# Kernel optimization log

Hardware: AMD Instinct MI355X
Metric: run time of the kernel (lower is better)

Reference implementation:

```python
import jax, jax.numpy as jnp
import numpy as np

N = 16384      # nodes
E = 524288     # edges (avg degree 32)
F_IN = 128     # input features
H1 = 256       # first_gcn_dimensions
H2 = 256       # second_gcn_dimensions
D1 = 64        # first_dense_neurons
D2 = 2         # second_dense_neurons (fixed by EYE=ones(2))


def setup_inputs() -> dict:
    key = jax.random.key(0)
    ks = jax.random.split(key, 8)
    w = lambda k, shp: (jax.random.normal(k, shp, jnp.float32) * 0.05)
    return dict(
        features=jax.random.normal(ks[0], (N, F_IN), jnp.float32),
        edges=jax.random.randint(ks[1], (2, E), 0, N),
        W1=w(ks[2], (F_IN, H1)), b1=jnp.zeros((H1,), jnp.float32),
        W2=w(ks[3], (H1, H2)), b2=jnp.zeros((H2,), jnp.float32),
        fc1_w=w(ks[4], (D1, H2)), fc1_b=jnp.zeros((D1,), jnp.float32),
        fc2_w=w(ks[5], (D2, D1)), fc2_b=jnp.zeros((D2,), jnp.float32),
    )


def gcn_conv(x, W, b, src, dst, n):
    """PyG GCNConv: xW, add self-loops, symmetric D^-1/2 (A+I) D^-1/2 aggregation."""
    x = x @ W
    loops = jnp.arange(n)
    s = jnp.concatenate([src, loops])
    d = jnp.concatenate([dst, loops])
    deg = jax.ops.segment_sum(jnp.ones(s.shape, x.dtype), d, num_segments=n)
    dinv = jnp.where(deg > 0, jax.lax.rsqrt(deg), 0.0)
    msg = x[s] * (dinv[s] * dinv[d])[:, None]          # gather + scale
    return jax.ops.segment_sum(msg, d, num_segments=n) + b  # scatter-add


def reference(features, edges, W1, b1, W2, b2, fc1_w, fc1_b, fc2_w, fc2_b):
    n = features.shape[0]
    src, dst = edges[0], edges[1]
    h1 = jax.nn.relu(gcn_conv(features, W1, b1, src, dst, n))
    h2 = gcn_conv(h1, W2, b2, src, dst, n)                 # [N, H2]
    a1 = jnp.tanh(h2 @ fc1_w.T + fc1_b)                    # [N, D1]
    assignment = jax.nn.softmax(a1 @ fc2_w.T + fc2_b, axis=1)  # [N, 2]
    group_features = assignment.T @ h2                     # [2, H2]
    # to_dense_adj: dense NxN adjacency, duplicate edges accumulate
    adj = jnp.zeros((n, n), h2.dtype).at[src, dst].add(1.0)
    new_adj = assignment.T @ (adj @ assignment)            # [2, 2]
    positive = jnp.clip(group_features[0][None, :], -100.0, 100.0)
    negative = jnp.clip(group_features[1][None, :], -100.0, 100.0)
    # F.normalize(p=1, dim=1) with eps=1e-12
    denom = jnp.maximum(jnp.sum(jnp.abs(new_adj), axis=1, keepdims=True), 1e-12)
    norm_diag = jnp.diag(new_adj / denom)
    pos_penalty = jnp.mean((norm_diag - 1.0) ** 2)         # MSE vs ones(2)
    graph_embedding = jnp.mean(group_features, axis=0, keepdims=True)  # [1, H2]
    return (graph_embedding, positive, negative, pos_penalty)
```

## Files before the change

kernel.cpp:

```cpp
#include <hip/hip_runtime.h>
#include <hip/hip_bf16.h>
#include <math.h>

#define N_NODES 16384
#define N_EDGES 524288
#define F_IN 128
#define H1 256
#define H2 256
#define D1 64
#define NA_GRID 128
#define DEG_CAP 96

typedef __attribute__((ext_vector_type(8))) short short8;
typedef __attribute__((ext_vector_type(4))) float floatx4;
typedef unsigned short ushort_t;
typedef unsigned int uint_t;

__device__ inline float bf2f(ushort_t u) {
    union { uint_t i; float f; } v;
    v.i = ((uint_t)u) << 16;
    return v.f;
}
__device__ inline ushort_t f2bs(float x) {
    __hip_bfloat16 h = __float2bfloat16(x);
    return *reinterpret_cast<ushort_t*>(&h);
}

__global__ __launch_bounds__(256) void prep_fill(
    const int* __restrict__ src, const int* __restrict__ dst,
    const float* __restrict__ features, const float* __restrict__ W1,
    const float* __restrict__ W2, const float* __restrict__ fc1_w,
    int* __restrict__ cur, int* __restrict__ col, ushort_t* __restrict__ z,
    ushort_t* __restrict__ W1t, ushort_t* __restrict__ W2t,
    ushort_t* __restrict__ fc1bf) {
    int b = blockIdx.x, t = threadIdx.x;
    if (b < 2048) {
        int e = b * 256 + t;
        int d = dst[e];
        int pos = atomicAdd(&cur[d], 1);
        if (pos < DEG_CAP) col[d * DEG_CAP + pos] = src[e];
    } else if (b < 4096) {
        int idx = ((b - 2048) * 256 + t) * 4;
        float4 v = *(const float4*)&features[idx];
        uint2 p;
        p.x = (uint_t)f2bs(v.x) | ((uint_t)f2bs(v.y) << 16);
        p.y = (uint_t)f2bs(v.z) | ((uint_t)f2bs(v.w) << 16);
        *(uint2*)&z[idx] = p;
    } else if (b < 4224) {
        int idx = (b - 4096) * 256 + t;
        int n = idx >> 7, k = idx & 127;
        W1t[idx] = f2bs(W1[k * 256 + n]);
    } else if (b < 4480) {
        int idx = (b - 4224) * 256 + t;
        int n = idx >> 8, k = idx & 255;
        W2t[idx] = f2bs(W2[k * 256 + n]);
    } else {
        int idx = (b - 4480) * 256 + t;
        fc1bf[idx] = f2bs(fc1_w[idx]);
    }
}

__global__ __launch_bounds__(256) void fused_layer1(
    const ushort_t* __restrict__ zfeat, const int* __restrict__ cnt,
    const int* __restrict__ col, const float* __restrict__ b1,
    const ushort_t* __restrict__ W1t, const ushort_t* __restrict__ W2t,
    ushort_t* __restrict__ bufY) {
    __shared__ __align__(16) ushort_t Az[16 * 136];
    __shared__ __align__(16) ushort_t Ah[16 * 264];
    const int tid = threadIdx.x;
    const int lane = tid & 63;
    const int wave = tid >> 6;
    const int m = lane & 15;
    const int quad = lane >> 4;
    const int row0 = blockIdx.x * 16;

    for (int ii = 0; ii < 4; ++ii) {
        const int nl = wave * 4 + ii;
        const int node = __builtin_amdgcn_readfirstlane(row0 + nl);
        const int foff = lane * 2;
        const int deg = cnt[node];
        float dnode = rsqrtf((float)(deg + 1));
        uint_t self = *(const uint_t*)&zfeat[(size_t)node * 128 + foff];
        float a0 = dnode * bf2f((ushort_t)(self & 0xffff));
        float a1 = dnode * bf2f((ushort_t)(self >> 16));
        const int s0 = node * DEG_CAP;
        const int s1 = s0 + min(deg, DEG_CAP);
        int base = s0;
        for (; base + 8 <= s1; base += 8) {
            uint_t uu[8]; float dv[8];
            #pragma unroll
            for (int q = 0; q < 8; ++q) {
                int j = col[base + q];
                dv[q] = rsqrtf((float)(cnt[j] + 1));
                uu[q] = *(const uint_t*)&zfeat[(size_t)j * 128 + foff];
            }
            #pragma unroll
            for (int q = 0; q < 8; ++q) {
                a0 += dv[q] * bf2f((ushort_t)(uu[q] & 0xffff));
                a1 += dv[q] * bf2f((ushort_t)(uu[q] >> 16));
            }
        }
        for (; base < s1; ++base) {
            int j = col[base];
            float dv = rsqrtf((float)(cnt[j] + 1));
            uint_t u = *(const uint_t*)&zfeat[(size_t)j * 128 + foff];
            a0 += dv * bf2f((ushort_t)(u & 0xffff));
            a1 += dv * bf2f((ushort_t)(u >> 16));
        }
        *(uint_t*)&Az[nl * 136 + foff] =
            (uint_t)f2bs(a0 * dnode) | ((uint_t)f2bs(a1 * dnode) << 16);
    }
    __syncthreads();

    const int wcol0 = wave * 64;
    floatx4 acc[4];
    const floatx4 zero4 = {0.f, 0.f, 0.f, 0.f};
    #pragma unroll
    for (int j = 0; j < 4; ++j) acc[j] = zero4;
    #pragma unroll
    for (int k0 = 0; k0 < 128; k0 += 32) {
        short8 a = *(const short8*)&Az[m * 136 + k0 + quad * 8];
        #pragma unroll
        for (int j = 0; j < 4; ++j) {
            short8 bb = *(const short8*)
                &W1t[(size_t)(wcol0 + j * 16 + m) * 128 + k0 + quad * 8];
            acc[j] = __builtin_amdgcn_mfma_f32_16x16x32_bf16(a, bb, acc[j], 0, 0, 0);
        }
    }
    #pragma unroll
    for (int j = 0; j < 4; ++j) {
        int cg = wcol0 + j * 16 + m;
        float bv = b1[cg];
        #pragma unroll
        for (int r = 0; r < 4; ++r) {
            float v = fmaxf(acc[j][r] + bv, 0.0f);
            Ah[(quad * 4 + r) * 264 + cg] = f2bs(v);
        }
    }
    __syncthreads();

    #pragma unroll
    for (int j = 0; j < 4; ++j) acc[j] = zero4;
    #pragma unroll
    for (int k0 = 0; k0 < 256; k0 += 32) {
        short8 a = *(const short8*)&Ah[m * 264 + k0 + quad * 8];
        #pragma unroll
        for (int j = 0; j < 4; ++j) {
            short8 bb = *(const short8*)
                &W2t[(size_t)(wcol0 + j * 16 + m) * 256 + k0 + quad * 8];
            acc[j] = __builtin_amdgcn_mfma_f32_16x16x32_bf16(a, bb, acc[j], 0, 0, 0);
        }
    }
    float rs4[4];
    #pragma unroll
    for (int r = 0; r < 4; ++r)
        rs4[r] = rsqrtf((float)(cnt[row0 + quad * 4 + r] + 1));
    #pragma unroll
    for (int j = 0; j < 4; ++j) {
        int cg = wcol0 + j * 16 + m;
        #pragma unroll
        for (int r = 0; r < 4; ++r)
            bufY[(size_t)(row0 + quad * 4 + r) * 256 + cg] = f2bs(acc[j][r] * rs4[r]);
    }
}

__global__ __launch_bounds__(256) void fused_assign(
    const ushort_t* __restrict__ bufY, const int* __restrict__ cnt,
    const int* __restrict__ col, const float* __restrict__ b2,
    const ushort_t* __restrict__ fc1bf, const float* __restrict__ fc1_b,
    const float* __restrict__ fc2_w, const float* __restrict__ fc2_b,
    float* __restrict__ assign, float* __restrict__ gfr) {
    __shared__ __align__(16) ushort_t Ah[16 * 264];
    __shared__ float sha[16][65];
    __shared__ float sas0[16], sas1[16];
    const int tid = threadIdx.x;
    const int lane = tid & 63;
    const int wave = tid >> 6;
    const int m = lane & 15;
    const int quad = lane >> 4;
    const int row0 = blockIdx.x * 16;

    for (int ii = 0; ii < 4; ++ii) {
        const int nl = wave * 4 + ii;
        const int node = __builtin_amdgcn_readfirstlane(row0 + nl);
        const int foff = lane * 4;
        const int deg = cnt[node];
        float a0, a1, a2, a3;
        {
            uint2 u = *(const uint2*)&bufY[(size_t)node * 256 + foff];
            a0 = bf2f((ushort_t)(u.x & 0xffff));
            a1 = bf2f((ushort_t)(u.x >> 16));
            a2 = bf2f((ushort_t)(u.y & 0xffff));
            a3 = bf2f((ushort_t)(u.y >> 16));
        }
        const int s0 = node * DEG_CAP;
        const int s1 = s0 + min(deg, DEG_CAP);
        int base = s0;
        for (; base + 8 <= s1; base += 8) {
            uint2 uu[8];
            #pragma unroll
            for (int q = 0; q < 8; ++q) {
                int j = col[base + q];
                uu[q] = *(const uint2*)&bufY[(size_t)j * 256 + foff];
            }
            #pragma unroll
            for (int q = 0; q < 8; ++q) {
                a0 += bf2f((ushort_t)(uu[q].x & 0xffff));
                a1 += bf2f((ushort_t)(uu[q].x >> 16));
                a2 += bf2f((ushort_t)(uu[q].y & 0xffff));
                a3 += bf2f((ushort_t)(uu[q].y >> 16));
            }
        }
        for (; base < s1; ++base) {
            int j = col[base];
            uint2 u = *(const uint2*)&bufY[(size_t)j * 256 + foff];
            a0 += bf2f((ushort_t)(u.x & 0xffff));
            a1 += bf2f((ushort_t)(u.x >> 16));
            a2 += bf2f((ushort_t)(u.y & 0xffff));
            a3 += bf2f((ushort_t)(u.y >> 16));
        }
        float di = rsqrtf((float)(deg + 1));
        uint2 pk;
        pk.x = (uint_t)f2bs(a0 * di + b2[foff + 0]) |
               ((uint_t)f2bs(a1 * di + b2[foff + 1]) << 16);
        pk.y = (uint_t)f2bs(a2 * di + b2[foff + 2]) |
               ((uint_t)f2bs(a3 * di + b2[foff + 3]) << 16);
        *(uint2*)&Ah[nl * 264 + foff] = pk;
    }
    __syncthreads();

    floatx4 acc = {0.f, 0.f, 0.f, 0.f};
    #pragma unroll
    for (int k0 = 0; k0 < 256; k0 += 32) {
        short8 a = *(const short8*)&Ah[m * 264 + k0 + quad * 8];
        short8 bb = *(const short8*)
            &fc1bf[(size_t)(wave * 16 + m) * 256 + k0 + quad * 8];
        acc = __builtin_amdgcn_mfma_f32_16x16x32_bf16(a, bb, acc, 0, 0, 0);
    }
    {
        int cg = wave * 16 + m;
        float bv = fc1_b[cg];
        #pragma unroll
        for (int r = 0; r < 4; ++r)
            sha[quad * 4 + r][cg] = tanhf(acc[r] + bv);
    }
    __syncthreads();

    if (tid < 16) {
        float p0 = fc2_b[0], p1 = fc2_b[1];
        #pragma unroll 8
        for (int t = 0; t < 64; ++t) {
            float a = sha[tid][t];
            p0 += a * fc2_w[t];
            p1 += a * fc2_w[64 + t];
        }
        float mx = fmaxf(p0, p1);
        float e0 = expf(p0 - mx), e1 = expf(p1 - mx);
        float inv = 1.0f / (e0 + e1);
        float2 as; as.x = e0 * inv; as.y = e1 * inv;
        *(float2*)&assign[(row0 + tid) * 2] = as;
        sas0[tid] = as.x; sas1[tid] = as.y;
    }
    __syncthreads();

    float acc0 = 0.f, acc1 = 0.f;
    #pragma unroll
    for (int i = 0; i < 16; ++i) {
        float h = bf2f(Ah[i * 264 + tid]);
        acc0 += sas0[i] * h;
        acc1 += sas1[i] * h;
    }
    float* gfc = gfr + (blockIdx.x & 3) * 512;
    atomicAdd(&gfc[tid], acc0);
    atomicAdd(&gfc[256 + tid], acc1);
}

__global__ __launch_bounds__(256) void newadj_fin(
    const int* __restrict__ src, const int* __restrict__ dst,
    const float* __restrict__ assign, float* __restrict__ napart,
    int* __restrict__ cntt, const float* __restrict__ gfr,
    float* __restrict__ out) {
    __shared__ float red[4][4];
    __shared__ int sticket;
    const int tid = threadIdx.x;
    const int b = blockIdx.x;
    const int lane = tid & 63;
    const int wave = tid >> 6;

    float a00 = 0.f, a01 = 0.f, a10 = 0.f, a11 = 0.f;
    for (int e = b * 256 + tid; e < N_EDGES; e += NA_GRID * 256) {
        int s = src[e], d = dst[e];
        float s0 = assign[s * 2], s1 = assign[s * 2 + 1];
        float d0 = assign[d * 2], d1 = assign[d * 2 + 1];
        a00 += s0 * d0; a01 += s0 * d1; a10 += s1 * d0; a11 += s1 * d1;
    }
    #pragma unroll
    for (int off = 32; off; off >>= 1) {
        a00 += __shfl_down(a00, off);
        a01 += __shfl_down(a01, off);
        a10 += __shfl_down(a10, off);
        a11 += __shfl_down(a11, off);
    }
    if (lane == 0) {
        red[wave][0] = a00; red[wave][1] = a01;
        red[wave][2] = a10; red[wave][3] = a11;
    }
    __syncthreads();
    if (tid < 4) {
        float v = red[0][tid] + red[1][tid] + red[2][tid] + red[3][tid];
        __hip_atomic_store(&napart[b * 4 + tid], v, __ATOMIC_RELEASE,
                           __HIP_MEMORY_SCOPE_AGENT);
    }
    __syncthreads();
    if (tid == 0)
        sticket = __hip_atomic_fetch_add(cntt, 1, __ATOMIC_ACQ_REL,
                                         __HIP_MEMORY_SCOPE_AGENT);
    __syncthreads();
    if (sticket != NA_GRID - 1) return;

    float acc = 0.f;
    for (int i = lane; i < NA_GRID; i += 64)
        acc += __hip_atomic_load(&napart[i * 4 + wave], __ATOMIC_RELAXED,
                                 __HIP_MEMORY_SCOPE_AGENT);
    #pragma unroll
    for (int off = 32; off; off >>= 1) acc += __shfl_down(acc, off);
    __shared__ float na[4];
    if (lane == 0) na[wave] = acc;
    __syncthreads();
    float g0 = gfr[tid] + gfr[512 + tid] + gfr[1024 + tid] + gfr[1536 + tid];
    float g1 = gfr[256 + tid] + gfr[768 + tid] + gfr[1280 + tid] + gfr[1792 + tid];
    out[tid] = 0.5f * (g0 + g1);
    out[256 + tid] = fminf(fmaxf(g0, -100.f), 100.f);
    out[512 + tid] = fminf(fmaxf(g1, -100.f), 100.f);
    if (tid == 0) {
        float n00 = na[0], n01 = na[1], n10 = na[2], n11 = na[3];
        float den0 = fmaxf(fabsf(n00) + fabsf(n01), 1e-12f);
        float den1 = fmaxf(fabsf(n10) + fabsf(n11), 1e-12f);
        float x0 = n00 / den0 - 1.0f;
        float x1 = n11 / den1 - 1.0f;
        out[768] = 0.5f * (x0 * x0 + x1 * x1);
    }
}


extern "C" void kernel_launch(void* const* d_in, const int* in_sizes, int n_in,
                              void* d_out, int out_size, void* d_ws, size_t ws_size,
                              hipStream_t stream) {
    const float* features = (const float*)d_in[0];
    const int* edges = (const int*)d_in[1];
    const int* src = edges;
    const int* dst = edges + N_EDGES;
    const float* W1 = (const float*)d_in[2];
    const float* b1 = (const float*)d_in[3];
    const float* W2 = (const float*)d_in[4];
    const float* b2 = (const float*)d_in[5];
    const float* fc1_w = (const float*)d_in[6];
    const float* fc1_b = (const float*)d_in[7];
    const float* fc2_w = (const float*)d_in[8];
    const float* fc2_b = (const float*)d_in[9];
    float* out = (float*)d_out;

    char* ws = (char*)d_ws;
    auto carve = [&](size_t bytes) {
        void* q = (void*)ws;
        ws += (bytes + 255) & ~(size_t)255;
        return q;
    };
    int* cur = (int*)carve(N_NODES * 4);
    float* gfr = (float*)carve(4 * 512 * 4);
    int* cnt_na = (int*)carve(256);
    int* col = (int*)carve((size_t)N_NODES * DEG_CAP * 4);
    float* assign = (float*)carve(N_NODES * 2 * 4);
    float* napart = (float*)carve(NA_GRID * 4 * 4);
    ushort_t* fc1bf = (ushort_t*)carve(64 * 256 * 2);
    ushort_t* zfeat = (ushort_t*)carve((size_t)N_NODES * F_IN * 2);
    ushort_t* W1t = (ushort_t*)carve(256 * 128 * 2);
    ushort_t* W2t = (ushort_t*)carve(256 * 256 * 2);
    ushort_t* bufY = (ushort_t*)carve((size_t)N_NODES * 256 * 2);

    hipMemsetAsync(cur, 0, N_NODES * 4 + 4 * 512 * 4 + 256, stream);

    prep_fill<<<4544, 256, 0, stream>>>(src, dst, features, W1, W2, fc1_w,
                                        cur, col, zfeat, W1t, W2t, fc1bf);
    fused_layer1<<<N_NODES / 16, 256, 0, stream>>>(
        zfeat, cur, col, b1, W1t, W2t, bufY);
    fused_assign<<<N_NODES / 16, 256, 0, stream>>>(
        bufY, cur, col, b2, fc1bf, fc1_b, fc2_w, fc2_b, assign, gfr);
    newadj_fin<<<NA_GRID, 256, 0, stream>>>(src, dst, assign, napart,
                                            cnt_na, gfr, out);
}
```

Measured before the change: 209.6 us.

## Prescale features by source degree norm and halve nodes per block

```diff
diff --git a/kernel.cpp b/kernel.cpp
--- a/kernel.cpp
+++ b/kernel.cpp
@@ -10,6 +10,7 @@
 #define D1 64
 #define NA_GRID 128
 #define DEG_CAP 96
+#define NPB 8
 
 typedef __attribute__((ext_vector_type(8))) short short8;
 typedef __attribute__((ext_vector_type(4))) float floatx4;
@@ -26,11 +27,18 @@
     return *reinterpret_cast<ushort_t*>(&h);
 }
 
+__global__ __launch_bounds__(256) void hist_kernel(
+    const int* __restrict__ dst, int* __restrict__ cnt) {
+    int e = blockIdx.x * 256 + threadIdx.x;
+    atomicAdd(&cnt[dst[e]], 1);
+}
+
 __global__ __launch_bounds__(256) void prep_fill(
     const int* __restrict__ src, const int* __restrict__ dst,
     const float* __restrict__ features, const float* __restrict__ W1,
     const float* __restrict__ W2, const float* __restrict__ fc1_w,
-    int* __restrict__ cur, int* __restrict__ col, ushort_t* __restrict__ z,
+    const int* __restrict__ cnt, int* __restrict__ cur,
+    int* __restrict__ col, ushort_t* __restrict__ z,
     ushort_t* __restrict__ W1t, ushort_t* __restrict__ W2t,
     ushort_t* __restrict__ fc1bf) {
     int b = blockIdx.x, t = threadIdx.x;
@@ -41,10 +49,11 @@
         if (pos < DEG_CAP) col[d * DEG_CAP + pos] = src[e];
     } else if (b < 4096) {
         int idx = ((b - 2048) * 256 + t) * 4;
+        float di = rsqrtf((float)(cnt[idx >> 7] + 1));
         float4 v = *(const float4*)&features[idx];
         uint2 p;
-        p.x = (uint_t)f2bs(v.x) | ((uint_t)f2bs(v.y) << 16);
-        p.y = (uint_t)f2bs(v.z) | ((uint_t)f2bs(v.w) << 16);
+        p.x = (uint_t)f2bs(v.x * di) | ((uint_t)f2bs(v.y * di) << 16);
+        p.y = (uint_t)f2bs(v.z * di) | ((uint_t)f2bs(v.w * di) << 16);
         *(uint2*)&z[idx] = p;
     } else if (b < 4224) {
         int idx = (b - 4096) * 256 + t;
@@ -72,41 +81,39 @@
     const int wave = tid >> 6;
     const int m = lane & 15;
     const int quad = lane >> 4;
-    const int row0 = blockIdx.x * 16;
-
-    for (int ii = 0; ii < 4; ++ii) {
-        const int nl = wave * 4 + ii;
+    const int row0 = blockIdx.x * NPB;
+
+    for (int ii = 0; ii < 2; ++ii) {
+        const int nl = wave * 2 + ii;
         const int node = __builtin_amdgcn_readfirstlane(row0 + nl);
         const int foff = lane * 2;
         const int deg = cnt[node];
-        float dnode = rsqrtf((float)(deg + 1));
         uint_t self = *(const uint_t*)&zfeat[(size_t)node * 128 + foff];
-        float a0 = dnode * bf2f((ushort_t)(self & 0xffff));
-        float a1 = dnode * bf2f((ushort_t)(self >> 16));
+        float a0 = bf2f((ushort_t)(self & 0xffff));
+        float a1 = bf2f((ushort_t)(self >> 16));
         const int s0 = node * DEG_CAP;
         const int s1 = s0 + min(deg, DEG_CAP);
         int base = s0;
         for (; base + 8 <= s1; base += 8) {
-            uint_t uu[8]; float dv[8];
+            uint_t uu[8];
             #pragma unroll
             for (int q = 0; q < 8; ++q) {
                 int j = col[base + q];
-                dv[q] = rsqrtf((float)(cnt[j] + 1));
                 uu[q] = *(const uint_t*)&zfeat[(size_t)j * 128 + foff];
             }
             #pragma unroll
             for (int q = 0; q < 8; ++q) {
-                a0 += dv[q] * bf2f((ushort_t)(uu[q] & 0xffff));
-                a1 += dv[q] * bf2f((ushort_t)(uu[q] >> 16));
+                a0 += bf2f((ushort_t)(uu[q] & 0xffff));
+                a1 += bf2f((ushort_t)(uu[q] >> 16));
             }
         }
         for (; base < s1; ++base) {
             int j = col[base];
-            float dv = rsqrtf((float)(cnt[j] + 1));
             uint_t u = *(const uint_t*)&zfeat[(size_t)j * 128 + foff];
-            a0 += dv * bf2f((ushort_t)(u & 0xffff));
-            a1 += dv * bf2f((ushort_t)(u >> 16));
-        }
+            a0 += bf2f((ushort_t)(u & 0xffff));
+            a1 += bf2f((ushort_t)(u >> 16));
+        }
+        float dnode = rsqrtf((float)(deg + 1));
         *(uint_t*)&Az[nl * 136 + foff] =
             (uint_t)f2bs(a0 * dnode) | ((uint_t)f2bs(a1 * dnode) << 16);
     }
@@ -127,14 +134,16 @@
             acc[j] = __builtin_amdgcn_mfma_f32_16x16x32_bf16(a, bb, acc[j], 0, 0, 0);
         }
     }
-    #pragma unroll
-    for (int j = 0; j < 4; ++j) {
-        int cg = wcol0 + j * 16 + m;
-        float bv = b1[cg];
-        #pragma unroll
-        for (int r = 0; r < 4; ++r) {
-            float v = fmaxf(acc[j][r] + bv, 0.0f);
-            Ah[(quad * 4 + r) * 264 + cg] = f2bs(v);
+    if (quad < 2) {
+        #pragma unroll
+        for (int j = 0; j < 4; ++j) {
+            int cg = wcol0 + j * 16 + m;
+            float bv = b1[cg];
+            #pragma unroll
+            for (int r = 0; r < 4; ++r) {
+                float v = fmaxf(acc[j][r] + bv, 0.0f);
+                Ah[(quad * 4 + r) * 264 + cg] = f2bs(v);
+            }
         }
     }
     __syncthreads();
@@ -151,16 +160,19 @@
             acc[j] = __builtin_amdgcn_mfma_f32_16x16x32_bf16(a, bb, acc[j], 0, 0, 0);
         }
     }
-    float rs4[4];
-    #pragma unroll
-    for (int r = 0; r < 4; ++r)
-        rs4[r] = rsqrtf((float)(cnt[row0 + quad * 4 + r] + 1));
-    #pragma unroll
-    for (int j = 0; j < 4; ++j) {
-        int cg = wcol0 + j * 16 + m;
+    if (quad < 2) {
+        float rs4[4];
         #pragma unroll
         for (int r = 0; r < 4; ++r)
-            bufY[(size_t)(row0 + quad * 4 + r) * 256 + cg] = f2bs(acc[j][r] * rs4[r]);
+            rs4[r] = rsqrtf((float)(cnt[row0 + quad * 4 + r] + 1));
+        #pragma unroll
+        for (int j = 0; j < 4; ++j) {
+            int cg = wcol0 + j * 16 + m;
+            #pragma unroll
+            for (int r = 0; r < 4; ++r)
+                bufY[(size_t)(row0 + quad * 4 + r) * 256 + cg] =
+                    f2bs(acc[j][r] * rs4[r]);
+        }
     }
 }
 
@@ -171,17 +183,17 @@
     const float* __restrict__ fc2_w, const float* __restrict__ fc2_b,
     float* __restrict__ assign, float* __restrict__ gfr) {
     __shared__ __align__(16) ushort_t Ah[16 * 264];
-    __shared__ float sha[16][65];
-    __shared__ float sas0[16], sas1[16];
+    __shared__ float sha[8][65];
+    __shared__ float sas0[8], sas1[8];
     const int tid = threadIdx.x;
     const int lane = tid & 63;
     const int wave = tid >> 6;
     const int m = lane & 15;
     const int quad = lane >> 4;
-    const int row0 = blockIdx.x * 16;
-
-    for (int ii = 0; ii < 4; ++ii) {
-        const int nl = wave * 4 + ii;
+    const int row0 = blockIdx.x * NPB;
+
+    for (int ii = 0; ii < 2; ++ii) {
+        const int nl = wave * 2 + ii;
         const int node = __builtin_amdgcn_readfirstlane(row0 + nl);
         const int foff = lane * 4;
         const int deg = cnt[node];
@@ -237,7 +249,7 @@
             &fc1bf[(size_t)(wave * 16 + m) * 256 + k0 + quad * 8];
         acc = __builtin_amdgcn_mfma_f32_16x16x32_bf16(a, bb, acc, 0, 0, 0);
     }
-    {
+    if (quad < 2) {
         int cg = wave * 16 + m;
         float bv = fc1_b[cg];
         #pragma unroll
@@ -246,7 +258,7 @@
     }
     __syncthreads();
 
-    if (tid < 16) {
+    if (tid < NPB) {
         float p0 = fc2_b[0], p1 = fc2_b[1];
         #pragma unroll 8
         for (int t = 0; t < 64; ++t) {
@@ -265,7 +277,7 @@
 
     float acc0 = 0.f, acc1 = 0.f;
     #pragma unroll
-    for (int i = 0; i < 16; ++i) {
+    for (int i = 0; i < NPB; ++i) {
         float h = bf2f(Ah[i * 264 + tid]);
         acc0 += sas0[i] * h;
         acc1 += sas1[i] * h;
@@ -366,6 +378,7 @@
         ws += (bytes + 255) & ~(size_t)255;
         return q;
     };
+    int* cnt = (int*)carve(N_NODES * 4);
     int* cur = (int*)carve(N_NODES * 4);
     float* gfr = (float*)carve(4 * 512 * 4);
     int* cnt_na = (int*)carve(256);
@@ -378,14 +391,15 @@
     ushort_t* W2t = (ushort_t*)carve(256 * 256 * 2);
     ushort_t* bufY = (ushort_t*)carve((size_t)N_NODES * 256 * 2);
 
-    hipMemsetAsync(cur, 0, N_NODES * 4 + 4 * 512 * 4 + 256, stream);
-
+    hipMemsetAsync(cnt, 0, N_NODES * 4 * 2 + 4 * 512 * 4 + 256, stream);
+
+    hist_kernel<<<N_EDGES / 256, 256, 0, stream>>>(dst, cnt);
     prep_fill<<<4544, 256, 0, stream>>>(src, dst, features, W1, W2, fc1_w,
-                                        cur, col, zfeat, W1t, W2t, fc1bf);
-    fused_layer1<<<N_NODES / 16, 256, 0, stream>>>(
-        zfeat, cur, col, b1, W1t, W2t, bufY);
-    fused_assign<<<N_NODES / 16, 256, 0, stream>>>(
-        bufY, cur, col, b2, fc1bf, fc1_b, fc2_w, fc2_b, assign, gfr);
+                                        cnt, cur, col, zfeat, W1t, W2t, fc1bf);
+    fused_layer1<<<N_NODES / NPB, 256, 0, stream>>>(
+        zfeat, cnt, col, b1, W1t, W2t, bufY);
+    fused_assign<<<N_NODES / NPB, 256, 0, stream>>>(
+        bufY, cnt, col, b2, fc1bf, fc1_b, fc2_w, fc2_b, assign, gfr);
     newadj_fin<<<NA_GRID, 256, 0, stream>>>(src, dst, assign, napart,
                                             cnt_na, gfr, out);
 }
```

Result: slower. 240.6 us (+14.8%).
